# Performance work log

Measured on AMD Instinct MI355X. Metric: run time of the kernel, lower is better.

## Reference

```python
import jax, jax.numpy as jnp
import numpy as np


def setup_inputs() -> dict:
    key = jax.random.key(0)
    ks = jax.random.split(key, 7)
    M, B, I, O = 8, 4096, 2048, 2048
    init_std = 0.1
    mu_init, rho_init = 0.0, -7.0
    weight_mu = jnp.clip(mu_init + init_std * jax.random.normal(ks[0], (M, I, O), jnp.float32),
                         mu_init - 2 * init_std, mu_init + 2 * init_std)
    bias_mu = jnp.clip(mu_init + init_std * jax.random.normal(ks[1], (M, 1, O), jnp.float32),
                       mu_init - 2 * init_std, mu_init + 2 * init_std)
    weight_rho = rho_init + init_std * jax.random.normal(ks[2], (M, I, O), jnp.float32)
    bias_rho = rho_init + init_std * jax.random.normal(ks[3], (M, 1, O), jnp.float32)
    return {
        "x": jax.random.normal(ks[4], (M, B, I), jnp.float32),
        "weight_mu": weight_mu,
        "weight_rho": weight_rho,
        "bias_mu": bias_mu,
        "bias_rho": bias_rho,
        "eps_w": jax.random.normal(ks[5], (M, I, O), jnp.float32),
        "eps_b": jax.random.normal(ks[6], (M, 1, O), jnp.float32),
    }


def reference(x, weight_mu, weight_rho, bias_mu, bias_rho, eps_w, eps_b):
    # Reparameterized weight sampling: sigma = softplus(rho); w = mu + sigma * eps
    w = weight_mu + jax.nn.softplus(weight_rho) * eps_w          # [M, I, O]
    b = bias_mu + jax.nn.softplus(bias_rho) * eps_b              # [M, 1, O]
    # Per-ensemble-member batched matmul: [M, B, I] @ [M, I, O] -> [M, B, O]
    return jnp.einsum("mbi,mio->mbo", x, w) + b
```

## Files before the change

kernel.cpp:

```cpp
#include <hip/hip_runtime.h>
#include <hip/hip_bf16.h>

#define M_ENS 8
#define BB    4096
#define KK    2048
#define OO    2048

typedef __bf16 bf16x8 __attribute__((ext_vector_type(8)));
typedef float  f32x4  __attribute__((ext_vector_type(4)));

__device__ __forceinline__ unsigned short f2bf(float f) {
    __hip_bfloat16 h = __float2bfloat16(f);
    return __builtin_bit_cast(unsigned short, h);
}

__device__ __forceinline__ float softplus_f(float x) {
    return fmaxf(x, 0.f) + log1pf(__expf(-fabsf(x)));
}

typedef __attribute__((address_space(1))) unsigned int gu32;
typedef __attribute__((address_space(3))) unsigned int su32;
__device__ __forceinline__ void gload_lds16(const void* g, void* s) {
    __builtin_amdgcn_global_load_lds((gu32*)g, (su32*)s, 16, 0, 0);
}

#define TI  64
#define TO  64
#define LDT 72

__global__ __launch_bounds__(256) void prep_w(const float* __restrict__ mu,
                                              const float* __restrict__ rho,
                                              const float* __restrict__ eps,
                                              unsigned short* __restrict__ wT) {
    __shared__ __align__(16) unsigned short sT[TO * LDT];

    const int o0 = blockIdx.x * TO;
    const int i0 = blockIdx.y * TI;
    const int m  = blockIdx.z;
    const size_t base_in  = (size_t)m * KK * OO;
    const size_t base_out = (size_t)m * OO * KK;

    const int tid    = threadIdx.x;
    const int o_l    = tid & 63;
    const int i_base = (tid >> 6) * 16;

    union { unsigned short us[16]; uint4 q[2]; } pk;
#pragma unroll
    for (int j = 0; j < 16; ++j) {
        const size_t idx = base_in + (size_t)(i0 + i_base + j) * OO + (o0 + o_l);
        pk.us[j] = f2bf(fmaf(softplus_f(rho[idx]), eps[idx], mu[idx]));
    }
    *reinterpret_cast<uint4*>(&sT[o_l * LDT + i_base])     = pk.q[0];
    *reinterpret_cast<uint4*>(&sT[o_l * LDT + i_base + 8]) = pk.q[1];

    __syncthreads();

#pragma unroll
    for (int p = 0; p < 2; ++p) {
        const int o_w = p * 32 + (tid >> 3);
        const int i_c = (tid & 7) * 8;
        *reinterpret_cast<uint4*>(&wT[base_out + (size_t)(o0 + o_w) * KK + i0 + i_c]) =
            *reinterpret_cast<const uint4*>(&sT[o_w * LDT + i_c]);
    }
}

#define BM  128
#define BN  128
#define BKT 32
#define LDA 40

__global__ __launch_bounds__(256) void gemm_kernel(const float* __restrict__ x,
                                                   const unsigned short* __restrict__ wT,
                                                   const float* __restrict__ bmu,
                                                   const float* __restrict__ brho,
                                                   const float* __restrict__ beps,
                                                   float* __restrict__ out) {
    __shared__ __align__(16) unsigned short sB[BN * BKT];
    __shared__ __align__(16) unsigned short sA[BM * LDA];
    __shared__ float sBias[BN];

    const int tid = threadIdx.x;
    const int w   = tid >> 6;
    const int l   = tid & 63;
    const int lr  = l & 15;
    const int lq  = l >> 4;
    const int n0   = blockIdx.x * BN;
    const int row0 = blockIdx.y * BM;
    const int m    = blockIdx.z;

    const float*          xm  = x   + (size_t)m * BB * KK;
    const unsigned short* wTm = wT  + (size_t)m * OO * KK;
    float*                om  = out + (size_t)m * BB * OO;

    if (tid < BN) {
        const size_t bi = (size_t)m * OO + n0 + tid;
        sBias[tid] = fmaf(softplus_f(brho[bi]), beps[bi], bmu[bi]);
    }

    const int wm = w >> 1, wn = w & 1;

    f32x4 acc[4][4];
#pragma unroll
    for (int a = 0; a < 4; ++a)
#pragma unroll
        for (int b = 0; b < 4; ++b)
#pragma unroll
            for (int j = 0; j < 4; ++j) acc[a][b][j] = 0.f;

    const int bswz = ((l & 3) ^ ((l >> 3) & 3)) * 8;
    const unsigned short* gB0 = wTm + (size_t)(n0 + 16 * w + (l >> 2)) * KK + bswz;
    const unsigned short* gB1 = gB0 + (size_t)64 * KK;
    unsigned short* sBw0 = sB + w * 512;
    unsigned short* sBw1 = sB + 2048 + w * 512;

    const int arow = tid >> 1, ahalf = tid & 1;
    const float* gA = xm + (size_t)(row0 + arow) * KK + ahalf * 16;
    unsigned short* sAw = sA + arow * LDA + ahalf * 16;

    const int bq = (lq ^ ((lr >> 1) & 3)) * 8;

    for (int kt = 0; kt < KK / BKT; ++kt) {
        const int k0 = kt * BKT;

        gload_lds16(gB0 + k0, sBw0);
        gload_lds16(gB1 + k0, sBw1);

        const float4 f0 = *reinterpret_cast<const float4*>(gA + k0);
        const float4 f1 = *reinterpret_cast<const float4*>(gA + k0 + 4);
        const float4 f2 = *reinterpret_cast<const float4*>(gA + k0 + 8);
        const float4 f3 = *reinterpret_cast<const float4*>(gA + k0 + 12);
        union { unsigned short us[16]; uint4 q[2]; } pk;
        pk.us[0]  = f2bf(f0.x); pk.us[1]  = f2bf(f0.y); pk.us[2]  = f2bf(f0.z); pk.us[3]  = f2bf(f0.w);
        pk.us[4]  = f2bf(f1.x); pk.us[5]  = f2bf(f1.y); pk.us[6]  = f2bf(f1.z); pk.us[7]  = f2bf(f1.w);
        pk.us[8]  = f2bf(f2.x); pk.us[9]  = f2bf(f2.y); pk.us[10] = f2bf(f2.z); pk.us[11] = f2bf(f2.w);
        pk.us[12] = f2bf(f3.x); pk.us[13] = f2bf(f3.y); pk.us[14] = f2bf(f3.z); pk.us[15] = f2bf(f3.w);
        *reinterpret_cast<uint4*>(sAw)     = pk.q[0];
        *reinterpret_cast<uint4*>(sAw + 8) = pk.q[1];

        __syncthreads();

        bf16x8 af[4], bv[4];
#pragma unroll
        for (int a = 0; a < 4; ++a)
            af[a] = *reinterpret_cast<const bf16x8*>(&sA[(wm * 64 + a * 16 + lr) * LDA + lq * 8]);
#pragma unroll
        for (int b = 0; b < 4; ++b)
            bv[b] = *reinterpret_cast<const bf16x8*>(&sB[(wn * 64 + b * 16 + lr) * BKT + bq]);

#pragma unroll
        for (int a = 0; a < 4; ++a)
#pragma unroll
            for (int b = 0; b < 4; ++b)
                acc[a][b] = __builtin_amdgcn_mfma_f32_16x16x32_bf16(af[a], bv[b], acc[a][b], 0, 0, 0);

        __syncthreads();
    }

#pragma unroll
    for (int b = 0; b < 4; ++b) {
        const int col  = wn * 64 + b * 16 + lr;
        const float bias = sBias[col];
#pragma unroll
        for (int a = 0; a < 4; ++a) {
            const int rbase = row0 + wm * 64 + a * 16 + lq * 4;
            float* po = om + (size_t)rbase * OO + n0 + col;
#pragma unroll
            for (int j = 0; j < 4; ++j)
                po[(size_t)j * OO] = acc[a][b][j] + bias;
        }
    }
}

extern "C" void kernel_launch(void* const* d_in, const int* in_sizes, int n_in,
                              void* d_out, int out_size, void* d_ws, size_t ws_size,
                              hipStream_t stream) {
    const float* x    = (const float*)d_in[0];
    const float* wmu  = (const float*)d_in[1];
    const float* wrho = (const float*)d_in[2];
    const float* bmu  = (const float*)d_in[3];
    const float* brho = (const float*)d_in[4];
    const float* ew   = (const float*)d_in[5];
    const float* eb   = (const float*)d_in[6];
    float* out = (float*)d_out;

    unsigned short* wT = (unsigned short*)d_ws;

    prep_w<<<dim3(OO / TO, KK / TI, M_ENS), 256, 0, stream>>>(wmu, wrho, ew, wT);
    gemm_kernel<<<dim3(OO / BN, BB / BM, M_ENS), 256, 0, stream>>>(x, wT, bmu, brho, eb, out);
}
```

Baseline: 1.143 ms.

## Pre-convert x to bf16 and use pipelined 256x256 GEMM with async LDS loads

Adds a prep_x kernel that converts x to bf16 once in workspace, then a new 512-thread gemm8 kernel with 256x256 tiles, K-tile 64, and double-buffered global_load_lds staging for both operands. The K loop interleaves the next tile's loads with MFMA quarters, using explicit barriers, waitcnt and setprio, and remaps block indices to improve L2 reuse. This is meant to remove the per-iteration fp32 A conversion and to overlap memory traffic with matrix math. The cost is an extra pass over x, plus dependence on workspace size and on hand-tuned waitcnt counts, with the old kernel kept as a fallback.

Measured after the change: 938.3 us. 17.9% less time.

```diff
diff --git a/kernel.cpp b/kernel.cpp
--- a/kernel.cpp
+++ b/kernel.cpp
@@ -61,6 +61,141 @@
         const int i_c = (tid & 7) * 8;
         *reinterpret_cast<uint4*>(&wT[base_out + (size_t)(o0 + o_w) * KK + i0 + i_c]) =
             *reinterpret_cast<const uint4*>(&sT[o_w * LDT + i_c]);
+    }
+}
+
+__global__ __launch_bounds__(256) void prep_x(const float* __restrict__ x,
+                                              unsigned short* __restrict__ xb) {
+    const size_t i = ((size_t)blockIdx.x * 256 + threadIdx.x) * 8;
+    const float4 f0 = *reinterpret_cast<const float4*>(x + i);
+    const float4 f1 = *reinterpret_cast<const float4*>(x + i + 4);
+    union { unsigned short us[8]; uint4 q; } pk;
+    pk.us[0] = f2bf(f0.x); pk.us[1] = f2bf(f0.y); pk.us[2] = f2bf(f0.z); pk.us[3] = f2bf(f0.w);
+    pk.us[4] = f2bf(f1.x); pk.us[5] = f2bf(f1.y); pk.us[6] = f2bf(f1.z); pk.us[7] = f2bf(f1.w);
+    *reinterpret_cast<uint4*>(xb + i) = pk.q;
+}
+
+#define NKT (KK / 64)
+
+#define BAR()   asm volatile("s_barrier" ::: "memory")
+#define LGKM0() asm volatile("s_waitcnt lgkmcnt(0)" ::: "memory")
+#define SCHB()  __builtin_amdgcn_sched_barrier(0)
+#define PRIO1() __builtin_amdgcn_s_setprio(1)
+#define PRIO0() __builtin_amdgcn_s_setprio(0)
+
+#define RD_A(P, HALF, mf, ks) \
+    (*reinterpret_cast<const bf16x8*>(sLds + (P)*32768 + aoff + (HALF)*4096 + (mf)*1024 + ((ks) ? ck1 : ck0)))
+#define RD_B(P, nf, ks) \
+    (*reinterpret_cast<const bf16x8*>(sLds + (P)*32768 + boff + (nf)*1024 + ((ks) ? ck1 : ck0)))
+
+#define ISSUE_A(P, T, J) gload_lds16(gAl + (size_t)(T)*64 + (size_t)(J)*(64*KK), \
+                                     sLds + (P)*32768 + (J)*4096 + wofs)
+#define ISSUE_B(P, T, J) gload_lds16(gBl + (size_t)(T)*64 + (size_t)(J)*(64*KK), \
+                                     sLds + (P)*32768 + 16384 + (J)*4096 + wofs)
+
+#define MFMA_Q(MH, NH) \
+    _Pragma("unroll") \
+    for (int ks_ = 0; ks_ < 2; ++ks_) \
+        _Pragma("unroll") \
+        for (int mf_ = 0; mf_ < 4; ++mf_) \
+            _Pragma("unroll") \
+            for (int nf_ = 0; nf_ < 2; ++nf_) \
+                acc[(MH)*4 + mf_][(NH)*2 + nf_] = __builtin_amdgcn_mfma_f32_16x16x32_bf16( \
+                    af[mf_][ks_], bv[(NH)*2 + nf_][ks_], acc[(MH)*4 + mf_][(NH)*2 + nf_], 0, 0, 0);
+
+#define TILE(T, P) do { \
+    _Pragma("unroll") for (int m_ = 0; m_ < 4; ++m_) { \
+        af[m_][0] = RD_A(P, 0, m_, 0); af[m_][1] = RD_A(P, 0, m_, 1); } \
+    _Pragma("unroll") for (int n_ = 0; n_ < 2; ++n_) { \
+        bv[n_][0] = RD_B(P, n_, 0); bv[n_][1] = RD_B(P, n_, 1); } \
+    if ((T) + 1 < NKT) { ISSUE_A((P)^1, (T)+1, 0); ISSUE_A((P)^1, (T)+1, 1); } \
+    BAR(); LGKM0(); SCHB(); PRIO1(); MFMA_Q(0, 0); PRIO0(); BAR(); \
+    _Pragma("unroll") for (int n_ = 0; n_ < 2; ++n_) { \
+        bv[2+n_][0] = RD_B(P, 2+n_, 0); bv[2+n_][1] = RD_B(P, 2+n_, 1); } \
+    if ((T) + 1 < NKT) { ISSUE_A((P)^1, (T)+1, 2); ISSUE_A((P)^1, (T)+1, 3); } \
+    BAR(); LGKM0(); SCHB(); PRIO1(); MFMA_Q(0, 1); PRIO0(); BAR(); \
+    _Pragma("unroll") for (int m_ = 0; m_ < 4; ++m_) { \
+        af[m_][0] = RD_A(P, 1, m_, 0); af[m_][1] = RD_A(P, 1, m_, 1); } \
+    if ((T) + 2 < NKT) { ISSUE_B(P, (T)+2, 0); ISSUE_B(P, (T)+2, 1); } \
+    BAR(); LGKM0(); SCHB(); PRIO1(); MFMA_Q(1, 0); PRIO0(); BAR(); \
+    if ((T) + 2 < NKT) { ISSUE_B(P, (T)+2, 2); ISSUE_B(P, (T)+2, 3); \
+                         asm volatile("s_waitcnt vmcnt(4)" ::: "memory"); } \
+    else               { asm volatile("s_waitcnt vmcnt(0)" ::: "memory"); } \
+    BAR(); SCHB(); PRIO1(); MFMA_Q(1, 1); PRIO0(); BAR(); \
+} while (0)
+
+__global__ __launch_bounds__(512, 2) void gemm8(const unsigned short* __restrict__ xb,
+                                                const unsigned short* __restrict__ wT,
+                                                const float* __restrict__ bmu,
+                                                const float* __restrict__ brho,
+                                                const float* __restrict__ beps,
+                                                float* __restrict__ out) {
+    __shared__ __align__(16) unsigned short sLds[65536];
+
+    const int tid = threadIdx.x;
+    const int w   = tid >> 6;
+    const int l   = tid & 63;
+    const int lr  = l & 15;
+    const int lq  = l >> 4;
+    const int wm  = w >> 2;
+    const int wn  = w & 3;
+    const int m   = blockIdx.y;
+
+    const int b    = blockIdx.x;
+    const int swz  = (b & 7) * 16 + (b >> 3);
+    const int n0   = (swz & 7) * 256;
+    const int row0 = (swz >> 3) * 256;
+
+    const unsigned short* xbm = xb + (size_t)m * BB * KK;
+    const unsigned short* wTm = wT + (size_t)m * OO * KK;
+
+    const int srow = w * 8 + (l >> 3);
+    const int sgc  = (l & 7) ^ (l >> 3);
+    const unsigned short* gAl = xbm + (size_t)(row0 + srow) * KK + sgc * 8;
+    const unsigned short* gBl = wTm + (size_t)(n0 + srow) * KK + sgc * 8;
+    const int wofs = w * 512;
+
+    const int h   = lr & 7;
+    const int u   = lq ^ (h & 3);
+    const int ck0 = (((h & 4)) | u) * 8;
+    const int ck1 = ((4 ^ (h & 4)) | u) * 8;
+    const int aoff = (wm * 128 + lr) * 64;
+    const int boff = 16384 + (wn * 64 + lr) * 64;
+
+    f32x4 acc[8][4];
+#pragma unroll
+    for (int a = 0; a < 8; ++a)
+#pragma unroll
+        for (int c = 0; c < 4; ++c)
+#pragma unroll
+            for (int j = 0; j < 4; ++j) acc[a][c][j] = 0.f;
+
+    bf16x8 af[4][2], bv[4][2];
+
+    ISSUE_A(0, 0, 0); ISSUE_A(0, 0, 1); ISSUE_A(0, 0, 2); ISSUE_A(0, 0, 3);
+    ISSUE_B(0, 0, 0); ISSUE_B(0, 0, 1); ISSUE_B(0, 0, 2); ISSUE_B(0, 0, 3);
+    ISSUE_B(1, 1, 0); ISSUE_B(1, 1, 1); ISSUE_B(1, 1, 2); ISSUE_B(1, 1, 3);
+    asm volatile("s_waitcnt vmcnt(4)" ::: "memory");
+    BAR();
+
+    for (int t2 = 0; t2 < NKT; t2 += 2) {
+        TILE(t2, 0);
+        TILE(t2 + 1, 1);
+    }
+
+    const size_t obase = (size_t)m * BB * OO;
+#pragma unroll
+    for (int nf = 0; nf < 4; ++nf) {
+        const int col = n0 + wn * 64 + nf * 16 + lr;
+        const size_t bi = (size_t)m * OO + col;
+        const float bias = fmaf(softplus_f(brho[bi]), beps[bi], bmu[bi]);
+#pragma unroll
+        for (int mf = 0; mf < 8; ++mf) {
+            float* po = out + obase + (size_t)(row0 + wm * 128 + mf * 16 + lq * 4) * OO + col;
+#pragma unroll
+            for (int j = 0; j < 4; ++j)
+                po[(size_t)j * OO] = acc[mf][nf][j] + bias;
+        }
     }
 }
 
@@ -103,9 +238,9 @@
 #pragma unroll
     for (int a = 0; a < 4; ++a)
 #pragma unroll
-        for (int b = 0; b < 4; ++b)
-#pragma unroll
-            for (int j = 0; j < 4; ++j) acc[a][b][j] = 0.f;
+        for (int c = 0; c < 4; ++c)
+#pragma unroll
+            for (int j = 0; j < 4; ++j) acc[a][c][j] = 0.f;
 
     const int bswz = ((l & 3) ^ ((l >> 3) & 3)) * 8;
     const unsigned short* gB0 = wTm + (size_t)(n0 + 16 * w + (l >> 2)) * KK + bswz;
@@ -121,7 +256,6 @@
 
     for (int kt = 0; kt < KK / BKT; ++kt) {
         const int k0 = kt * BKT;
-
         gload_lds16(gB0 + k0, sBw0);
         gload_lds16(gB1 + k0, sBw1);
 
@@ -139,26 +273,26 @@
 
         __syncthreads();
 
-        bf16x8 af[4], bv[4];
+        bf16x8 afv[4], bvv[4];
 #pragma unroll
         for (int a = 0; a < 4; ++a)
-            af[a] = *reinterpret_cast<const bf16x8*>(&sA[(wm * 64 + a * 16 + lr) * LDA + lq * 8]);
-#pragma unroll
-        for (int b = 0; b < 4; ++b)
-            bv[b] = *reinterpret_cast<const bf16x8*>(&sB[(wn * 64 + b * 16 + lr) * BKT + bq]);
+            afv[a] = *reinterpret_cast<const bf16x8*>(&sA[(wm * 64 + a * 16 + lr) * LDA + lq * 8]);
+#pragma unroll
+        for (int c = 0; c < 4; ++c)
+            bvv[c] = *reinterpret_cast<const bf16x8*>(&sB[(wn * 64 + c * 16 + lr) * BKT + bq]);
 
 #pragma unroll
         for (int a = 0; a < 4; ++a)
 #pragma unroll
-            for (int b = 0; b < 4; ++b)
-                acc[a][b] = __builtin_amdgcn_mfma_f32_16x16x32_bf16(af[a], bv[b], acc[a][b], 0, 0, 0);
+            for (int c = 0; c < 4; ++c)
+                acc[a][c] = __builtin_amdgcn_mfma_f32_16x16x32_bf16(afv[a], bvv[c], acc[a][c], 0, 0, 0);
 
         __syncthreads();
     }
 
 #pragma unroll
-    for (int b = 0; b < 4; ++b) {
-        const int col  = wn * 64 + b * 16 + lr;
+    for (int c = 0; c < 4; ++c) {
+        const int col  = wn * 64 + c * 16 + lr;
         const float bias = sBias[col];
 #pragma unroll
         for (int a = 0; a < 4; ++a) {
@@ -166,7 +300,7 @@
             float* po = om + (size_t)rbase * OO + n0 + col;
 #pragma unroll
             for (int j = 0; j < 4; ++j)
-                po[(size_t)j * OO] = acc[a][b][j] + bias;
+                po[(size_t)j * OO] = acc[a][c][j] + bias;
         }
     }
 }
@@ -183,8 +317,18 @@
     const float* eb   = (const float*)d_in[6];
     float* out = (float*)d_out;
 
+    const size_t needW = (size_t)M_ENS * OO * KK;
+    const size_t needX = (size_t)M_ENS * BB * KK;
+
     unsigned short* wT = (unsigned short*)d_ws;
 
     prep_w<<<dim3(OO / TO, KK / TI, M_ENS), 256, 0, stream>>>(wmu, wrho, ew, wT);
-    gemm_kernel<<<dim3(OO / BN, BB / BM, M_ENS), 256, 0, stream>>>(x, wT, bmu, brho, eb, out);
-}
+
+    if (ws_size >= (needW + needX) * sizeof(unsigned short)) {
+        unsigned short* xbuf = wT + needW;
+        prep_x<<<dim3((unsigned)(needX / 8 / 256)), 256, 0, stream>>>(x, xbuf);
+        gemm8<<<dim3((OO / 256) * (BB / 256), M_ENS), 512, 0, stream>>>(xbuf, wT, bmu, brho, eb, out);
+    } else {
+        gemm_kernel<<<dim3(OO / BN, BB / BM, M_ENS), 256, 0, stream>>>(x, wT, bmu, brho, eb, out);
+    }
+}
```
